# Kernel optimization log

Hardware: AMD Instinct MI355X
Metric: run time of the kernel (lower is better)

The kernel has to match this reference:

```python
import jax, jax.numpy as jnp
import numpy as np

WIN = (7, 7, 7)
DIM = 192
HEADS = 6
N = WIN[0] * WIN[1] * WIN[2]  # 343
TABLE = (2 * WIN[0] - 1) * (2 * WIN[1] - 1) * (2 * WIN[2] - 1)  # 2197


def _relative_position_index():
    d, h, w = WIN
    coords = np.stack(np.meshgrid(np.arange(d), np.arange(h), np.arange(w), indexing='ij'))
    flat = coords.reshape(3, -1)  # [3, N]
    rel = flat[:, :, None] - flat[:, None, :]  # [3, N, N]
    rel = rel.transpose(1, 2, 0).copy()
    rel[:, :, 0] += d - 1
    rel[:, :, 1] += h - 1
    rel[:, :, 2] += w - 1
    rel[:, :, 0] *= (2 * h - 1) * (2 * w - 1)
    rel[:, :, 1] *= 2 * w - 1
    return jnp.asarray(rel.sum(-1), dtype=jnp.int32)  # [N, N]


def setup_inputs() -> dict:
    key = jax.random.key(0)
    ks = jax.random.split(key, 8)
    b = 256
    nw = 64
    x = jax.random.normal(ks[0], (b, N, DIM), dtype=jnp.float32)
    mask = jax.random.normal(ks[1], (nw, N, N), dtype=jnp.float32)
    s = 1.0 / np.sqrt(DIM)
    wq = jax.random.normal(ks[2], (DIM, DIM), dtype=jnp.float32) * s
    wk = jax.random.normal(ks[3], (DIM, DIM), dtype=jnp.float32) * s
    wv = jax.random.normal(ks[4], (DIM, DIM), dtype=jnp.float32) * s
    rel_table = jax.random.normal(ks[5], (TABLE, HEADS), dtype=jnp.float32) * 0.02
    proj_w = jax.random.normal(ks[6], (DIM, DIM), dtype=jnp.float32) * s
    proj_b = jnp.zeros((DIM,), dtype=jnp.float32)
    return {"x": x, "mask": mask, "wq": wq, "wk": wk, "wv": wv,
            "rel_table": rel_table, "proj_w": proj_w, "proj_b": proj_b}


def reference(x, mask, wq, wk, wv, rel_table, proj_w, proj_b):
    b, n, c = x.shape
    hd = c // HEADS
    scale = hd ** (-0.5)
    rel_idx = _relative_position_index()[:n, :n]  # [n, n] int32
    # torch Linear: x @ W.T  -> [b, H, n, hd]
    q = (x @ wq.T).reshape(b, n, HEADS, hd).transpose(0, 2, 1, 3) * scale
    k = (x @ wk.T).reshape(b, n, HEADS, hd).transpose(0, 2, 1, 3)
    v = (x @ wv.T).reshape(b, n, HEADS, hd).transpose(0, 2, 1, 3)
    attn = jnp.einsum('bhqd,bhkd->bhqk', q, k)  # [b, H, n, n]
    bias = rel_table[rel_idx.reshape(-1)].reshape(n, n, HEADS)
    attn = attn + bias.transpose(2, 0, 1)[None]
    nw = mask.shape[0]
    attn = attn.reshape(b // nw, nw, HEADS, n, n) + mask[None, :, None]
    attn = attn.reshape(b, HEADS, n, n)
    attn = jax.nn.softmax(attn, axis=-1)
    out = jnp.einsum('bhqk,bhkd->bhqd', attn, v).transpose(0, 2, 1, 3).reshape(b, n, c)
    return out @ proj_w.T + proj_b
```

## Files before the change

### kernel.cpp

```cpp
#include <hip/hip_runtime.h>
#include <hip/hip_bf16.h>

typedef __bf16 bf16_t;
typedef __bf16 bf16x8 __attribute__((ext_vector_type(8)));
typedef float f32x4 __attribute__((ext_vector_type(4)));

#define N_TOK 343
#define NP    352
#define DIM   192
#define HEADS 6
#define HD    32
#define BATCH 256
#define NW    64
#define MROWS (BATCH * N_TOK)
#define LOG2E 1.4426950408889634f

static __device__ __forceinline__ f32x4 mfma_bf16(bf16x8 a, bf16x8 b, f32x4 c) {
    return __builtin_amdgcn_mfma_f32_16x16x32_bf16(a, b, c, 0, 0, 0);
}

__global__ __launch_bounds__(256) void wprep_kernel(
    const float* __restrict__ wq, const float* __restrict__ wk,
    const float* __restrict__ wv, const float* __restrict__ pw,
    bf16_t* __restrict__ wb)
{
    int t = blockIdx.x * 256 + threadIdx.x;
    int mat = t / 4608, off = (t % 4608) * 8;
    const float* src = (mat == 0) ? wq : ((mat == 1) ? wk : ((mat == 2) ? wv : pw));
    const float scale = (mat == 0) ? (0.17677669529663687f * LOG2E) : 1.0f;
    float4 f0 = *(const float4*)(src + off);
    float4 f1 = *(const float4*)(src + off + 4);
    bf16x8 o;
    o[0]=(bf16_t)(f0.x*scale); o[1]=(bf16_t)(f0.y*scale);
    o[2]=(bf16_t)(f0.z*scale); o[3]=(bf16_t)(f0.w*scale);
    o[4]=(bf16_t)(f1.x*scale); o[5]=(bf16_t)(f1.y*scale);
    o[6]=(bf16_t)(f1.z*scale); o[7]=(bf16_t)(f1.w*scale);
    *(bf16x8*)(wb + mat * 36864 + off) = o;
}

__global__ __launch_bounds__(256) void qkv_kernel(
    const float* __restrict__ x, const bf16_t* __restrict__ wb,
    bf16_t* __restrict__ qo, bf16_t* __restrict__ ko, bf16_t* __restrict__ vo)
{
    __shared__ __align__(16) bf16_t xs[64 * 200];
    const int tid = threadIdx.x;
    const long m0 = (long)blockIdx.x * 64;
    for (int e = tid; e < 3072; e += 256) {
        int flat = e * 4;
        int row = flat / 192, col = flat - row * 192;
        float4 f = *(const float4*)(x + m0 * 192 + flat);
        bf16_t* dst = &xs[row * 200 + col];
        dst[0] = (bf16_t)f.x; dst[1] = (bf16_t)f.y;
        dst[2] = (bf16_t)f.z; dst[3] = (bf16_t)f.w;
    }
    __syncthreads();
    const int wave = tid >> 6, lane = tid & 63;
    const int g = lane >> 4, c = lane & 15;
    #pragma unroll 1
    for (int ct = wave; ct < 36; ct += 4) {
        const int mat = ct / 12, n0 = (ct % 12) * 16;
        bf16_t* O = (mat == 0) ? qo : ((mat == 1) ? ko : vo);
        const int hh = n0 >> 5, dd = (n0 & 31) + c;
        const bf16_t* wrow = wb + mat * 36864 + (n0 + c) * 192 + g * 8;
        bf16x8 bfrag[6];
        #pragma unroll
        for (int ks = 0; ks < 6; ks++) bfrag[ks] = *(const bf16x8*)(wrow + ks * 32);
        #pragma unroll
        for (int mt = 0; mt < 4; mt++) {
            f32x4 acc = {0.f, 0.f, 0.f, 0.f};
            #pragma unroll
            for (int ks = 0; ks < 6; ks++) {
                bf16x8 a = *(const bf16x8*)&xs[(mt * 16 + c) * 200 + ks * 32 + g * 8];
                acc = mfma_bf16(a, bfrag[ks], acc);
            }
            int mb = (int)m0 + mt * 16 + g * 4;
            #pragma unroll
            for (int i = 0; i < 4; i++) {
                int m = mb + i;
                int bb = m / 343;
                int tok = m - bb * 343;
                O[((long)(bb * 6 + hh) * 343 + tok) * 32 + dd] = (bf16_t)acc[i];
            }
        }
    }
}

__global__ void maskprep_kernel(const float* __restrict__ mask, bf16_t* __restrict__ mp) {
    long row = blockIdx.x;
    int t = threadIdx.x;
    if (t < NP) {
        float vv = 0.f;
        if (t < N_TOK) vv = __builtin_amdgcn_exp2f(mask[row * N_TOK + t] * LOG2E);
        mp[row * NP + t] = (bf16_t)vv;
    }
}

__global__ void biasprep_kernel(const float* __restrict__ rel_table, bf16_t* __restrict__ bp) {
    int r = blockIdx.x;
    int h = blockIdx.y;
    int j = threadIdx.x;
    if (j < NP) {
        float vv = 0.f;
        if (j < N_TOK) {
            int dr = r / 49, hr = (r / 7) % 7, wr = r % 7;
            int dj = j / 49, hj = (j / 7) % 7, wj = j % 7;
            int idx = (dr - dj + 6) * 169 + (hr - hj + 6) * 13 + (wr - wj + 6);
            vv = __builtin_amdgcn_exp2f(rel_table[idx * HEADS + h] * LOG2E);
        }
        bp[((long)h * N_TOK + r) * NP + j] = (bf16_t)vv;
    }
}

__global__ __launch_bounds__(256) void attn_kernel(
    const bf16_t* __restrict__ q, const bf16_t* __restrict__ k,
    const bf16_t* __restrict__ v, const bf16_t* __restrict__ maskp,
    const bf16_t* __restrict__ biasp, bf16_t* __restrict__ aout)
{
    __shared__ __align__(16) bf16_t K_lds[NP * 40];
    __shared__ __align__(16) bf16_t Vt_lds[HD * 360];
    const int f = blockIdx.x;
    const int xcd = f & 7;
    const int idx8 = f >> 3;
    const int pair = xcd * 48 + (idx8 >> 2);
    const int rep  = idx8 & 3;
    const int w = pair / 6, h = pair - (pair / 6) * 6;
    const int b = rep * 64 + w;
    const int tid = threadIdx.x;
    const bf16_t* kbase = k + (long)(b * 6 + h) * N_TOK * HD;
    const bf16_t* vbase = v + (long)(b * 6 + h) * N_TOK * HD;
    const bf16_t* qb    = q + (long)(b * 6 + h) * N_TOK * HD;

    for (int idx = tid; idx < 1408; idx += 256) {
        int j = idx >> 2, dcol = (idx & 3) * 8;
        int blk = j >> 5, w32 = j & 31;
        int gg = w32 >> 3, rem = w32 & 7, tt = rem >> 2, ii = rem & 3;
        int lr = blk * 32 + tt * 16 + gg * 4 + ii;
        bf16x8 val = {};
        if (j < N_TOK) val = *(const bf16x8*)(kbase + idx * 8);
        *(bf16x8*)&K_lds[lr * 40 + dcol] = val;
    }
    for (int idx = tid; idx < 1408; idx += 256) {
        int j = idx >> 2, dcol = (idx & 3) * 8;
        if (j < N_TOK) {
            bf16x8 val = *(const bf16x8*)(vbase + idx * 8);
            #pragma unroll
            for (int ii = 0; ii < 8; ii++) Vt_lds[(dcol + ii) * 360 + j] = val[ii];
        } else {
            #pragma unroll
            for (int ii = 0; ii < 8; ii++) Vt_lds[(dcol + ii) * 360 + j] = (bf16_t)0.f;
        }
    }
    __syncthreads();

    const int wave = tid >> 6, lane = tid & 63;
    const int g = lane >> 4, c = lane & 15;
    const bf16_t* mbase = maskp + (long)w * N_TOK * NP;
    const bf16_t* bbase = biasp + (long)h * N_TOK * NP;

    for (int qt = wave; qt < 22; qt += 4) {
        const int rc = min(qt * 16 + c, N_TOK - 1);
        bf16x8 qf = *(const bf16x8*)(qb + (long)rc * HD + g * 8);
        const bf16_t* mrow = mbase + (long)rc * NP;
        const bf16_t* brow = bbase + (long)rc * NP;
        f32x4 olo = {0.f,0.f,0.f,0.f}, ohi = {0.f,0.f,0.f,0.f};
        float rs = 0.f;
        for (int jb = 0; jb < 11; jb++) {
            const int j0 = jb * 32 + g * 8;
            bf16x8 fm = *(const bf16x8*)(mrow + j0);
            bf16x8 fb = *(const bf16x8*)(brow + j0);
            bf16x8 k0 = *(const bf16x8*)&K_lds[(jb * 32 + c) * 40 + g * 8];
            bf16x8 k1 = *(const bf16x8*)&K_lds[(jb * 32 + 16 + c) * 40 + g * 8];
            const f32x4 z = {0.f,0.f,0.f,0.f};
            f32x4 s0 = mfma_bf16(k0, qf, z);
            f32x4 s1 = mfma_bf16(k1, qf, z);
            float p[8];
            #pragma unroll
            for (int e = 0; e < 4; e++) {
                p[e]     = __builtin_amdgcn_exp2f(s0[e]) * ((float)fm[e]     * (float)fb[e]);
                p[4 + e] = __builtin_amdgcn_exp2f(s1[e]) * ((float)fm[4 + e] * (float)fb[4 + e]);
            }
            #pragma unroll
            for (int e = 0; e < 8; e++) rs += p[e];
            bf16x8 pf;
            #pragma unroll
            for (int e = 0; e < 8; e++) pf[e] = (bf16_t)p[e];
            bf16x8 v0 = *(const bf16x8*)&Vt_lds[c * 360 + j0];
            bf16x8 v1 = *(const bf16x8*)&Vt_lds[(c + 16) * 360 + j0];
            olo = mfma_bf16(pf, v0, olo);
            ohi = mfma_bf16(pf, v1, ohi);
        }
        rs += __shfl_xor(rs, 16);
        rs += __shfl_xor(rs, 32);
        #pragma unroll
        for (int i = 0; i < 4; i++) {
            int row = qt * 16 + g * 4 + i;
            if (row < N_TOK) {
                float inv = 1.f / __shfl(rs, g * 4 + i);
                bf16_t* dst = aout + ((long)(b * 6 + h) * N_TOK + row) * HD;
                dst[c]      = (bf16_t)(olo[i] * inv);
                dst[c + 16] = (bf16_t)(ohi[i] * inv);
            }
        }
    }
}

__global__ __launch_bounds__(256) void proj_kernel(
    const bf16_t* __restrict__ A, const bf16_t* __restrict__ wb,
    const float* __restrict__ bias, float* __restrict__ out)
{
    __shared__ __align__(16) bf16_t xs[64 * 200];
    const int tid = threadIdx.x;
    const long m0 = (long)blockIdx.x * 64;
    for (int e = tid; e < 1536; e += 256) {
        int row = e / 24, col = (e % 24) * 8;
        int m = (int)m0 + row;
        int bb = m / 343;
        int tok = m - bb * 343;
        int hh = col >> 5, dd = col & 31;
        *(bf16x8*)&xs[row * 200 + col] =
            *(const bf16x8*)(A + ((long)(bb * 6 + hh) * 343 + tok) * 32 + dd);
    }
    __syncthreads();
    const int wave = tid >> 6, lane = tid & 63;
    const int g = lane >> 4, c = lane & 15;
    #pragma unroll 1
    for (int ct = wave; ct < 12; ct += 4) {
        const int n0 = ct * 16;
        const bf16_t* wrow = wb + 3 * 36864 + (n0 + c) * 192 + g * 8;
        bf16x8 bfrag[6];
        #pragma unroll
        for (int ks = 0; ks < 6; ks++) bfrag[ks] = *(const bf16x8*)(wrow + ks * 32);
        const float bv = bias[n0 + c];
        #pragma unroll
        for (int mt = 0; mt < 4; mt++) {
            f32x4 acc = {0.f, 0.f, 0.f, 0.f};
            #pragma unroll
            for (int ks = 0; ks < 6; ks++) {
                bf16x8 a = *(const bf16x8*)&xs[(mt * 16 + c) * 200 + ks * 32 + g * 8];
                acc = mfma_bf16(a, bfrag[ks], acc);
            }
            long mb = m0 + mt * 16 + g * 4;
            #pragma unroll
            for (int i = 0; i < 4; i++)
                out[(mb + i) * 192 + n0 + c] = acc[i] + bv;
        }
    }
}

extern "C" void kernel_launch(void* const* d_in, const int* in_sizes, int n_in,
                              void* d_out, int out_size, void* d_ws, size_t ws_size,
                              hipStream_t stream)
{
    const float* x         = (const float*)d_in[0];
    const float* mask      = (const float*)d_in[1];
    const float* wq        = (const float*)d_in[2];
    const float* wk        = (const float*)d_in[3];
    const float* wv        = (const float*)d_in[4];
    const float* rel_table = (const float*)d_in[5];
    const float* proj_w    = (const float*)d_in[6];
    const float* proj_b    = (const float*)d_in[7];
    float* out = (float*)d_out;

    char* ws = (char*)d_ws;
    const size_t SZ = (size_t)MROWS * DIM * 2;
    bf16_t* q_ws  = (bf16_t*)(ws);
    bf16_t* k_ws  = (bf16_t*)(ws + SZ);
    bf16_t* v_ws  = (bf16_t*)(ws + 2 * SZ);
    bf16_t* a_ws  = (bf16_t*)(ws + 3 * SZ);
    bf16_t* mp_ws = (bf16_t*)(ws + 4 * SZ);
    bf16_t* bp_ws = (bf16_t*)(ws + 4 * SZ + (size_t)NW * N_TOK * NP * 2);
    bf16_t* wb_ws = (bf16_t*)(ws + 4 * SZ + (size_t)NW * N_TOK * NP * 2
                                 + (size_t)HEADS * N_TOK * NP * 2);

    hipLaunchKernelGGL(wprep_kernel, dim3(72), dim3(256), 0, stream,
                       wq, wk, wv, proj_w, wb_ws);
    hipLaunchKernelGGL(maskprep_kernel, dim3(NW * N_TOK), dim3(384), 0, stream, mask, mp_ws);
    hipLaunchKernelGGL(biasprep_kernel, dim3(N_TOK, HEADS), dim3(384), 0, stream,
                       rel_table, bp_ws);
    hipLaunchKernelGGL(qkv_kernel, dim3(1372), dim3(256), 0, stream,
                       x, wb_ws, q_ws, k_ws, v_ws);
    hipLaunchKernelGGL(attn_kernel, dim3(BATCH * HEADS), dim3(256), 0, stream,
                       q_ws, k_ws, v_ws, mp_ws, bp_ws, a_ws);
    hipLaunchKernelGGL(proj_kernel, dim3(1372), dim3(256), 0, stream,
                       a_ws, wb_ws, proj_b, out);
}
```

Baseline: 242.0 us.

## Store exp mask/bias in fp32, prefetch rows, compute row sums via MFMA

```diff
diff --git a/kernel.cpp b/kernel.cpp
--- a/kernel.cpp
+++ b/kernel.cpp
@@ -85,17 +85,17 @@
     }
 }
 
-__global__ void maskprep_kernel(const float* __restrict__ mask, bf16_t* __restrict__ mp) {
+__global__ void maskprep_kernel(const float* __restrict__ mask, float* __restrict__ mp) {
     long row = blockIdx.x;
     int t = threadIdx.x;
     if (t < NP) {
         float vv = 0.f;
         if (t < N_TOK) vv = __builtin_amdgcn_exp2f(mask[row * N_TOK + t] * LOG2E);
-        mp[row * NP + t] = (bf16_t)vv;
-    }
-}
-
-__global__ void biasprep_kernel(const float* __restrict__ rel_table, bf16_t* __restrict__ bp) {
+        mp[row * NP + t] = vv;
+    }
+}
+
+__global__ void biasprep_kernel(const float* __restrict__ rel_table, float* __restrict__ bp) {
     int r = blockIdx.x;
     int h = blockIdx.y;
     int j = threadIdx.x;
@@ -107,14 +107,14 @@
             int idx = (dr - dj + 6) * 169 + (hr - hj + 6) * 13 + (wr - wj + 6);
             vv = __builtin_amdgcn_exp2f(rel_table[idx * HEADS + h] * LOG2E);
         }
-        bp[((long)h * N_TOK + r) * NP + j] = (bf16_t)vv;
+        bp[((long)h * N_TOK + r) * NP + j] = vv;
     }
 }
 
 __global__ __launch_bounds__(256) void attn_kernel(
     const bf16_t* __restrict__ q, const bf16_t* __restrict__ k,
-    const bf16_t* __restrict__ v, const bf16_t* __restrict__ maskp,
-    const bf16_t* __restrict__ biasp, bf16_t* __restrict__ aout)
+    const bf16_t* __restrict__ v, const float* __restrict__ maskp,
+    const float* __restrict__ biasp, bf16_t* __restrict__ aout)
 {
     __shared__ __align__(16) bf16_t K_lds[NP * 40];
     __shared__ __align__(16) bf16_t Vt_lds[HD * 360];
@@ -154,48 +154,59 @@
 
     const int wave = tid >> 6, lane = tid & 63;
     const int g = lane >> 4, c = lane & 15;
-    const bf16_t* mbase = maskp + (long)w * N_TOK * NP;
-    const bf16_t* bbase = biasp + (long)h * N_TOK * NP;
+    const float* mbase = maskp + (long)w * N_TOK * NP;
+    const float* bbase = biasp + (long)h * N_TOK * NP;
+    bf16x8 ones;
+    #pragma unroll
+    for (int e = 0; e < 8; e++) ones[e] = (bf16_t)1.0f;
 
     for (int qt = wave; qt < 22; qt += 4) {
         const int rc = min(qt * 16 + c, N_TOK - 1);
         bf16x8 qf = *(const bf16x8*)(qb + (long)rc * HD + g * 8);
-        const bf16_t* mrow = mbase + (long)rc * NP;
-        const bf16_t* brow = bbase + (long)rc * NP;
+        const float* mrow = mbase + (long)rc * NP + g * 8;
+        const float* brow = bbase + (long)rc * NP + g * 8;
         f32x4 olo = {0.f,0.f,0.f,0.f}, ohi = {0.f,0.f,0.f,0.f};
-        float rs = 0.f;
+        f32x4 osum = {0.f,0.f,0.f,0.f};
+        float4 fmA0 = *(const float4*)(mrow);
+        float4 fmA1 = *(const float4*)(mrow + 4);
+        float4 fbA0 = *(const float4*)(brow);
+        float4 fbA1 = *(const float4*)(brow + 4);
         for (int jb = 0; jb < 11; jb++) {
             const int j0 = jb * 32 + g * 8;
-            bf16x8 fm = *(const bf16x8*)(mrow + j0);
-            bf16x8 fb = *(const bf16x8*)(brow + j0);
+            float4 fm0 = fmA0, fm1 = fmA1, fb0 = fbA0, fb1 = fbA1;
+            const int jn = (jb < 10) ? (jb * 32 + 32) : (jb * 32);
+            fmA0 = *(const float4*)(mrow + jn);
+            fmA1 = *(const float4*)(mrow + jn + 4);
+            fbA0 = *(const float4*)(brow + jn);
+            fbA1 = *(const float4*)(brow + jn + 4);
             bf16x8 k0 = *(const bf16x8*)&K_lds[(jb * 32 + c) * 40 + g * 8];
             bf16x8 k1 = *(const bf16x8*)&K_lds[(jb * 32 + 16 + c) * 40 + g * 8];
             const f32x4 z = {0.f,0.f,0.f,0.f};
             f32x4 s0 = mfma_bf16(k0, qf, z);
             f32x4 s1 = mfma_bf16(k1, qf, z);
             float p[8];
-            #pragma unroll
-            for (int e = 0; e < 4; e++) {
-                p[e]     = __builtin_amdgcn_exp2f(s0[e]) * ((float)fm[e]     * (float)fb[e]);
-                p[4 + e] = __builtin_amdgcn_exp2f(s1[e]) * ((float)fm[4 + e] * (float)fb[4 + e]);
-            }
-            #pragma unroll
-            for (int e = 0; e < 8; e++) rs += p[e];
+            p[0] = __builtin_amdgcn_exp2f(s0[0]) * (fm0.x * fb0.x);
+            p[1] = __builtin_amdgcn_exp2f(s0[1]) * (fm0.y * fb0.y);
+            p[2] = __builtin_amdgcn_exp2f(s0[2]) * (fm0.z * fb0.z);
+            p[3] = __builtin_amdgcn_exp2f(s0[3]) * (fm0.w * fb0.w);
+            p[4] = __builtin_amdgcn_exp2f(s1[0]) * (fm1.x * fb1.x);
+            p[5] = __builtin_amdgcn_exp2f(s1[1]) * (fm1.y * fb1.y);
+            p[6] = __builtin_amdgcn_exp2f(s1[2]) * (fm1.z * fb1.z);
+            p[7] = __builtin_amdgcn_exp2f(s1[3]) * (fm1.w * fb1.w);
             bf16x8 pf;
             #pragma unroll
             for (int e = 0; e < 8; e++) pf[e] = (bf16_t)p[e];
             bf16x8 v0 = *(const bf16x8*)&Vt_lds[c * 360 + j0];
             bf16x8 v1 = *(const bf16x8*)&Vt_lds[(c + 16) * 360 + j0];
-            olo = mfma_bf16(pf, v0, olo);
-            ohi = mfma_bf16(pf, v1, ohi);
-        }
-        rs += __shfl_xor(rs, 16);
-        rs += __shfl_xor(rs, 32);
+            olo  = mfma_bf16(pf, v0, olo);
+            ohi  = mfma_bf16(pf, v1, ohi);
+            osum = mfma_bf16(pf, ones, osum);
+        }
         #pragma unroll
         for (int i = 0; i < 4; i++) {
             int row = qt * 16 + g * 4 + i;
             if (row < N_TOK) {
-                float inv = 1.f / __shfl(rs, g * 4 + i);
+                float inv = 1.f / osum[i];
                 bf16_t* dst = aout + ((long)(b * 6 + h) * N_TOK + row) * HD;
                 dst[c]      = (bf16_t)(olo[i] * inv);
                 dst[c + 16] = (bf16_t)(ohi[i] * inv);
@@ -267,10 +278,10 @@
     bf16_t* k_ws  = (bf16_t*)(ws + SZ);
     bf16_t* v_ws  = (bf16_t*)(ws + 2 * SZ);
     bf16_t* a_ws  = (bf16_t*)(ws + 3 * SZ);
-    bf16_t* mp_ws = (bf16_t*)(ws + 4 * SZ);
-    bf16_t* bp_ws = (bf16_t*)(ws + 4 * SZ + (size_t)NW * N_TOK * NP * 2);
-    bf16_t* wb_ws = (bf16_t*)(ws + 4 * SZ + (size_t)NW * N_TOK * NP * 2
-                                 + (size_t)HEADS * N_TOK * NP * 2);
+    float*  mp_ws = (float*)(ws + 4 * SZ);
+    float*  bp_ws = (float*)(ws + 4 * SZ + (size_t)NW * N_TOK * NP * 4);
+    bf16_t* wb_ws = (bf16_t*)(ws + 4 * SZ + (size_t)NW * N_TOK * NP * 4
+                                 + (size_t)HEADS * N_TOK * NP * 4);
 
     hipLaunchKernelGGL(wprep_kernel, dim3(72), dim3(256), 0, stream,
                        wq, wk, wv, proj_w, wb_ws);
```

Measured after the change: 313.7 us. +29.6%, slower.
